# Kernel optimization log

Hardware: AMD Instinct MI355X
Metric: run time of the kernel (lower is better)

## Reference

```python
import jax, jax.numpy as jnp
import numpy as np

N = 100_000      # nodes
E = 500_000      # bonds
DN = 128         # dim_node_embedding
DB = 64          # dim_bond_embedding
NTOK = 4         # num_bond_token
DIN = 2 * DN + 2 * DB  # 384
LEAKY = 0.001
LN_EPS = 1e-5
DIST_MAX = 20.0
STEP = 0.5


def _lrelu(v):
    return jnp.where(v >= 0, v, LEAKY * v)


def _layernorm(v, w, b):
    m = v.mean(-1, keepdims=True)
    var = ((v - m) ** 2).mean(-1, keepdims=True)
    return (v - m) / jnp.sqrt(var + LN_EPS) * w + b


def setup_inputs() -> dict:
    key = jax.random.key(0)
    ks = jax.random.split(key, 20)
    x = jax.random.normal(ks[0], (N, 3), dtype=jnp.float32) * 3.0
    pos = jax.random.normal(ks[1], (N, 3), dtype=jnp.float32)
    node_embedding = jax.random.normal(ks[2], (N, DN), dtype=jnp.float32)
    i0 = jax.random.randint(ks[3], (E,), 0, N)
    off = jax.random.randint(ks[4], (E,), 1, N)  # nonzero -> no self-bonds
    bond_index = jnp.stack([i0, (i0 + off) % N], axis=1).astype(jnp.int32)
    bond_types = jax.random.randint(ks[5], (E,), 0, NTOK).astype(jnp.int32)
    s = 0.02
    params = dict(
        bond_emb=jax.random.normal(ks[6], (NTOK, DB), dtype=jnp.float32),
        W0=jax.random.normal(ks[7], (DIN, DN), dtype=jnp.float32) * s,
        b0=jnp.zeros((DN,), jnp.float32),
        W1=jax.random.normal(ks[8], (DN, DN), dtype=jnp.float32) * s,
        b1=jnp.zeros((DN,), jnp.float32),
        ln1_w=jnp.ones((DN,), jnp.float32),
        ln1_b=jnp.zeros((DN,), jnp.float32),
        W2=jax.random.normal(ks[9], (DN, DN), dtype=jnp.float32) * s,
        b2=jnp.zeros((DN,), jnp.float32),
        ln2_w=jnp.ones((DN,), jnp.float32),
        ln2_b=jnp.zeros((DN,), jnp.float32),
        Wo=jax.random.normal(ks[10], (DN, 2), dtype=jnp.float32) * s,
        bo=jnp.zeros((2,), jnp.float32),
    )
    return dict(x=x, pos=pos, node_embedding=node_embedding,
                bond_index=bond_index, bond_types=bond_types, **params)


def reference(x, pos, node_embedding, bond_index, bond_types,
              bond_emb, W0, b0, W1, b1, ln1_w, ln1_b,
              W2, b2, ln2_w, ln2_b, Wo, bo):
    i = bond_index[:, 0]
    j = bond_index[:, 1]

    # ---- BondLength geometry ----
    diff = x[i] - x[j]                                   # [E,3]
    dist = jnp.linalg.norm(diff, axis=-1, keepdims=True)  # [E,1]
    u = diff / dist                                       # [E,3] unit j->i? (i-j)/d
    direction = jnp.stack([u, -u], axis=-1)               # [E,3,2]

    # ---- Smearing (gaussian RBF + overflow bin, normalized) ----
    offset = jnp.linspace(0.0, DIST_MAX, DB - 1, dtype=jnp.float32)  # [63]
    delta = DIST_MAX / (DB - 2)
    coeff = -0.5 / (delta * delta)
    rbf = jnp.exp(coeff * (dist - offset) ** 2)            # [E,63]
    ovf = (dist >= DIST_MAX).astype(x.dtype)               # [E,1]
    smear = jnp.concatenate([rbf, ovf], axis=-1)           # [E,64]
    smear = smear / smear.sum(axis=-1, keepdims=True)

    # ---- Edge MLP (LeakyMLP, num_layer=2, dim_end=2) ----
    feat = jnp.concatenate(
        [node_embedding[i], node_embedding[j], bond_emb[bond_types], smear],
        axis=-1)                                           # [E,384]
    h = _lrelu(feat @ W0 + b0)
    h = _lrelu(_layernorm(h @ W1 + b1, ln1_w, ln1_b))
    h = _lrelu(_layernorm(h @ W2 + b2, ln2_w, ln2_b))
    force = h @ Wo + bo                                    # [E,2]

    # ---- position update (scatter-add) ----
    update = force[:, None, :] * direction                 # [E,3,2]
    pos = pos.at[i].add(STEP * update[..., 0])
    pos = pos.at[j].add(STEP * update[..., 1])
    return pos
```

## Files before the change

kernel.cpp:

```cpp
#include <hip/hip_runtime.h>
#include <stdint.h>

#define N_EDGES 500000
#define N_NODES 100000

typedef __attribute__((ext_vector_type(8))) short short8;
typedef __attribute__((ext_vector_type(4))) float floatx4;

__device__ __forceinline__ uint16_t f2bf(float f) {
  union { float f; uint32_t u; } cv; cv.f = f;
  uint32_t u = cv.u;
  return (uint16_t)((u + 0x7FFFu + ((u >> 16) & 1u)) >> 16);
}
__device__ __forceinline__ float bf2f(uint16_t h) {
  union { uint32_t u; float f; } cv; cv.u = ((uint32_t)h) << 16; return cv.f;
}
__device__ __forceinline__ float lrelu(float v) { return v >= 0.0f ? v : 0.001f * v; }

__global__ void prep0_kernel(const float* __restrict__ W0, const float* __restrict__ b0,
                             const float* __restrict__ W1, const float* __restrict__ W2,
                             const float* __restrict__ bemb,
                             uint16_t* __restrict__ w0ab, uint16_t* __restrict__ w0c,
                             uint16_t* __restrict__ w1f, uint16_t* __restrict__ w2f,
                             float* __restrict__ be0f) {
  int id = blockIdx.x * 256 + threadIdx.x;
  if (id < 32768) {
    int f = id;
    int j = f & 7, lane = (f >> 3) & 63, ntt = (f >> 9) & 15, ks = f >> 13;
    int k = ks * 32 + (lane >> 4) * 8 + j;
    int row = (ntt < 8) ? k : (128 + k);
    int col = (ntt & 7) * 16 + (lane & 15);
    w0ab[f] = f2bf(W0[row * 128 + col]);
  } else if (id < 40960) {
    int f = id - 32768;
    int j = f & 7, lane = (f >> 3) & 63, nt = (f >> 9) & 7, ks = f >> 12;
    int k = ks * 32 + (lane >> 4) * 8 + j;
    w0c[f] = f2bf(W0[(320 + k) * 128 + nt * 16 + (lane & 15)]);
  } else if (id < 57344) {
    int f = id - 40960;
    int j = f & 7, lane = (f >> 3) & 63, nt = (f >> 9) & 7, ks = f >> 12;
    int k = ks * 32 + (lane >> 4) * 8 + j;
    w1f[f] = f2bf(W1[k * 128 + nt * 16 + (lane & 15)]);
  } else if (id < 73728) {
    int f = id - 57344;
    int j = f & 7, lane = (f >> 3) & 63, nt = (f >> 9) & 7, ks = f >> 12;
    int k = ks * 32 + (lane >> 4) * 8 + j;
    w2f[f] = f2bf(W2[k * 128 + nt * 16 + (lane & 15)]);
  } else if (id < 74240) {
    int t = id - 73728; int ty = t >> 7, n = t & 127;
    float s = b0[n];
    for (int kk = 0; kk < 64; ++kk) s += bemb[ty * 64 + kk] * W0[(256 + kk) * 128 + n];
    be0f[t] = s;
  }
}

__launch_bounds__(256, 3)
__global__ void prep_p_kernel(const float* __restrict__ nemb, const uint16_t* __restrict__ w0ab,
                              uint16_t* __restrict__ Pa, uint16_t* __restrict__ Pb) {
  __shared__ __align__(16) uint16_t aLds[4 * 16 * 136];
  const int tid = threadIdx.x;
  const int lane = tid & 63;
  const int wave = tid >> 6;
  const int n15 = lane & 15;
  const int quad = lane >> 4;
  uint16_t* myA = aLds + wave * (16 * 136);
  const int base = blockIdx.x * 64 + wave * 16;

  {
    const int le = lane >> 2, sub = lane & 3;
    int r = base + le; if (r >= N_NODES) r = N_NODES - 1;
    const float4* src = (const float4*)(nemb + (size_t)r * 128);
#pragma unroll
    for (int g = 0; g < 4; ++g) {
      float4 a = src[sub * 8 + g * 2], b = src[sub * 8 + g * 2 + 1];
      uint4 pk;
      pk.x = f2bf(a.x) | ((uint32_t)f2bf(a.y) << 16);
      pk.y = f2bf(a.z) | ((uint32_t)f2bf(a.w) << 16);
      pk.z = f2bf(b.x) | ((uint32_t)f2bf(b.y) << 16);
      pk.w = f2bf(b.z) | ((uint32_t)f2bf(b.w) << 16);
      *(uint4*)(myA + le * 136 + sub * 32 + g * 8) = pk;
    }
  }

  floatx4 acc[16];
#pragma unroll
  for (int t = 0; t < 16; ++t) acc[t] = (floatx4){0.f, 0.f, 0.f, 0.f};
#pragma unroll
  for (int ks = 0; ks < 4; ++ks) {
    short8 a = *(const short8*)(myA + n15 * 136 + ks * 32 + quad * 8);
#pragma unroll
    for (int ntt = 0; ntt < 16; ++ntt) {
      short8 b = *(const short8*)(w0ab + ((ks * 16 + ntt) * 64 + lane) * 8);
      acc[ntt] = __builtin_amdgcn_mfma_f32_16x16x32_bf16(a, b, acc[ntt], 0, 0, 0);
    }
  }

#pragma unroll
  for (int p = 0; p < 2; ++p) {
#pragma unroll
    for (int nt = 0; nt < 8; ++nt)
#pragma unroll
      for (int r = 0; r < 4; ++r)
        myA[(quad * 4 + r) * 136 + nt * 16 + n15] = f2bf(acc[p * 8 + nt][r]);
    const int le = lane >> 2, sub = lane & 3;
    int row = base + le;
    if (row < N_NODES) {
      uint16_t* dst = (p == 0 ? Pa : Pb) + (size_t)row * 128;
#pragma unroll
      for (int g = 0; g < 4; ++g)
        *(uint4*)(dst + sub * 32 + g * 8) =
            *(const uint4*)(myA + le * 136 + sub * 32 + g * 8);
    }
  }
}

__global__ void copy_pos_kernel(const float* __restrict__ pos, float* __restrict__ out, int n) {
  int id = blockIdx.x * 256 + threadIdx.x;
  if (id < n) out[id] = pos[id];
}

template <int NKS>
__device__ __forceinline__ void gemm_fw(const uint16_t* __restrict__ wf,
                                        const uint16_t* aRow, int lane, floatx4* acc) {
#pragma unroll
  for (int ks = 0; ks < NKS; ++ks) {
    short8 a = *(const short8*)(aRow + ks * 32);
#pragma unroll
    for (int nt = 0; nt < 8; ++nt) {
      short8 b = *(const short8*)(wf + ((ks * 8 + nt) * 64 + lane) * 8);
      acc[nt] = __builtin_amdgcn_mfma_f32_16x16x32_bf16(a, b, acc[nt], 0, 0, 0);
    }
  }
}

__launch_bounds__(256, 3)
__global__ void bond_mlp_kernel(const float* __restrict__ x,
                                const int* __restrict__ bidx, const int* __restrict__ btyp,
                                const uint16_t* __restrict__ Pa, const uint16_t* __restrict__ Pb,
                                const uint16_t* __restrict__ w0c, const uint16_t* __restrict__ w1f,
                                const uint16_t* __restrict__ w2f, const float* __restrict__ be0f,
                                const float* __restrict__ b1, const float* __restrict__ ln1w,
                                const float* __restrict__ ln1b,
                                const float* __restrict__ b2, const float* __restrict__ ln2w,
                                const float* __restrict__ ln2b,
                                const float* __restrict__ Wo, const float* __restrict__ bo,
                                float* __restrict__ out) {
  __shared__ __align__(16) uint16_t wlds[4 * 5312];
  __shared__ float u_lds[64][3];
  __shared__ int ij_lds[64][2];
  __shared__ int type_lds[64];

  const int tid = threadIdx.x;
  const int lane = tid & 63;
  const int wave = tid >> 6;
  const int n15 = lane & 15;
  const int quad = lane >> 4;

  uint16_t* base16 = wlds + wave * 5312;
  float* h0pre = (float*)base16;
  uint16_t* hA = base16;
  uint16_t* smearA = base16 + 4160;

  {
    const int le = lane >> 2, sub = lane & 3;
    const int lrow = le;
    const int ge = blockIdx.x * 64 + wave * 16 + le;
    const bool valid = ge < N_EDGES;
    int vi = 0, vj = 0, bt = 0;
    if (valid) { vi = bidx[2 * ge]; vj = bidx[2 * ge + 1]; bt = btyp[ge]; }
    float dx, dy, dz;
    if (valid) {
      dx = x[3 * vi]     - x[3 * vj];
      dy = x[3 * vi + 1] - x[3 * vj + 1];
      dz = x[3 * vi + 2] - x[3 * vj + 2];
    } else { dx = 1.0f; dy = 0.0f; dz = 0.0f; }
    float dist = sqrtf(dx * dx + dy * dy + dz * dz);
    float rinv = 1.0f / dist;
    if (sub == 0) {
      int gr = wave * 16 + lrow;
      u_lds[gr][0] = dx * rinv; u_lds[gr][1] = dy * rinv; u_lds[gr][2] = dz * rinv;
      ij_lds[gr][0] = vi; ij_lds[gr][1] = vj; type_lds[gr] = bt;
    }
    const uint4* pa = (const uint4*)(Pa + (size_t)vi * 128);
    const uint4* pb = (const uint4*)(Pb + (size_t)vj * 128);
    const float4* bb = (const float4*)(be0f + bt * 128);
#pragma unroll
    for (int g = 0; g < 4; ++g) {
      uint4 av = pa[sub * 4 + g];
      uint4 bv = pb[sub * 4 + g];
      float4 e0 = bb[sub * 8 + g * 2], e1 = bb[sub * 8 + g * 2 + 1];
      float4 s0, s1;
      s0.x = bf2f((uint16_t)(av.x & 0xFFFF)) + bf2f((uint16_t)(bv.x & 0xFFFF)) + e0.x;
      s0.y = bf2f((uint16_t)(av.x >> 16))    + bf2f((uint16_t)(bv.x >> 16))    + e0.y;
      s0.z = bf2f((uint16_t)(av.y & 0xFFFF)) + bf2f((uint16_t)(bv.y & 0xFFFF)) + e0.z;
      s0.w = bf2f((uint16_t)(av.y >> 16))    + bf2f((uint16_t)(bv.y >> 16))    + e0.w;
      s1.x = bf2f((uint16_t)(av.z & 0xFFFF)) + bf2f((uint16_t)(bv.z & 0xFFFF)) + e1.x;
      s1.y = bf2f((uint16_t)(av.z >> 16))    + bf2f((uint16_t)(bv.z >> 16))    + e1.y;
      s1.z = bf2f((uint16_t)(av.w & 0xFFFF)) + bf2f((uint16_t)(bv.w & 0xFFFF)) + e1.z;
      s1.w = bf2f((uint16_t)(av.w >> 16))    + bf2f((uint16_t)(bv.w >> 16))    + e1.w;
      *(float4*)(h0pre + lrow * 130 + sub * 32 + g * 8) = s0;
      *(float4*)(h0pre + lrow * 130 + sub * 32 + g * 8 + 4) = s1;
    }
    const float delta = 20.0f / 62.0f;
    const float coeff = -0.5f / (delta * delta);
    float sv[16]; float ssum = 0.0f;
#pragma unroll
    for (int t = 0; t < 16; ++t) {
      int kk = sub * 16 + t;
      float v;
      if (kk < 63) { float d = dist - (float)kk * delta; v = __expf(coeff * d * d); }
      else v = (dist >= 20.0f) ? 1.0f : 0.0f;
      sv[t] = v; ssum += v;
    }
    ssum += __shfl_xor(ssum, 1);
    ssum += __shfl_xor(ssum, 2);
    float sinv = 1.0f / ssum;
#pragma unroll
    for (int g = 0; g < 2; ++g) {
      uint4 pk;
      pk.x = f2bf(sv[g*8+0]*sinv) | ((uint32_t)f2bf(sv[g*8+1]*sinv) << 16);
      pk.y = f2bf(sv[g*8+2]*sinv) | ((uint32_t)f2bf(sv[g*8+3]*sinv) << 16);
      pk.z = f2bf(sv[g*8+4]*sinv) | ((uint32_t)f2bf(sv[g*8+5]*sinv) << 16);
      pk.w = f2bf(sv[g*8+6]*sinv) | ((uint32_t)f2bf(sv[g*8+7]*sinv) << 16);
      *(uint4*)(smearA + lrow * 72 + sub * 16 + g * 8) = pk;
    }
  }

  floatx4 acc[8];
#pragma unroll
  for (int nt = 0; nt < 8; ++nt)
#pragma unroll
    for (int r = 0; r < 4; ++r)
      acc[nt][r] = h0pre[(quad * 4 + r) * 130 + nt * 16 + n15];

  gemm_fw<2>(w0c, smearA + n15 * 72 + quad * 8, lane, acc);

#pragma unroll
  for (int nt = 0; nt < 8; ++nt)
#pragma unroll
    for (int r = 0; r < 4; ++r)
      hA[(quad * 4 + r) * 136 + nt * 16 + n15] = f2bf(lrelu(acc[nt][r]));

#pragma unroll
  for (int nt = 0; nt < 8; ++nt) acc[nt] = (floatx4){0.f, 0.f, 0.f, 0.f};
  gemm_fw<4>(w1f, hA + n15 * 136 + quad * 8, lane, acc);

  {
    float bv[8], wv[8], bb2[8];
#pragma unroll
    for (int nt = 0; nt < 8; ++nt) {
      int col = nt * 16 + n15;
      bv[nt] = b1[col]; wv[nt] = ln1w[col]; bb2[nt] = ln1b[col];
    }
    float s[4] = {0,0,0,0}, q[4] = {0,0,0,0};
#pragma unroll
    for (int nt = 0; nt < 8; ++nt)
#pragma unroll
      for (int r = 0; r < 4; ++r) { float v = acc[nt][r] + bv[nt]; s[r] += v; q[r] += v * v; }
#pragma unroll
    for (int m = 1; m <= 8; m <<= 1)
#pragma unroll
      for (int r = 0; r < 4; ++r) { s[r] += __shfl_xor(s[r], m); q[r] += __shfl_xor(q[r], m); }
    float mean[4], rstd[4];
#pragma unroll
    for (int r = 0; r < 4; ++r) {
      mean[r] = s[r] * (1.0f / 128.0f);
      float var = q[r] * (1.0f / 128.0f) - mean[r] * mean[r];
      rstd[r] = rsqrtf(var + 1e-5f);
    }
#pragma unroll
    for (int nt = 0; nt < 8; ++nt)
#pragma unroll
      for (int r = 0; r < 4; ++r) {
        float v = acc[nt][r] + bv[nt];
        float vn = (v - mean[r]) * rstd[r] * wv[nt] + bb2[nt];
        hA[(quad * 4 + r) * 136 + nt * 16 + n15] = f2bf(lrelu(vn));
      }
  }

#pragma unroll
  for (int nt = 0; nt < 8; ++nt) acc[nt] = (floatx4){0.f, 0.f, 0.f, 0.f};
  gemm_fw<4>(w2f, hA + n15 * 136 + quad * 8, lane, acc);

  {
    float bv[8], wv[8], bb2[8], wo0[8], wo1[8];
#pragma unroll
    for (int nt = 0; nt < 8; ++nt) {
      int col = nt * 16 + n15;
      bv[nt] = b2[col]; wv[nt] = ln2w[col]; bb2[nt] = ln2b[col];
      wo0[nt] = Wo[2 * col]; wo1[nt] = Wo[2 * col + 1];
    }
    float s[4] = {0,0,0,0}, q[4] = {0,0,0,0};
#pragma unroll
    for (int nt = 0; nt < 8; ++nt)
#pragma unroll
      for (int r = 0; r < 4; ++r) { float v = acc[nt][r] + bv[nt]; s[r] += v; q[r] += v * v; }
#pragma unroll
    for (int m = 1; m <= 8; m <<= 1)
#pragma unroll
      for (int r = 0; r < 4; ++r) { s[r] += __shfl_xor(s[r], m); q[r] += __shfl_xor(q[r], m); }
    float mean[4], rstd[4];
#pragma unroll
    for (int r = 0; r < 4; ++r) {
      mean[r] = s[r] * (1.0f / 128.0f);
      float var = q[r] * (1.0f / 128.0f) - mean[r] * mean[r];
      rstd[r] = rsqrtf(var + 1e-5f);
    }
    float f0[4] = {0,0,0,0}, f1[4] = {0,0,0,0};
#pragma unroll
    for (int nt = 0; nt < 8; ++nt)
#pragma unroll
      for (int r = 0; r < 4; ++r) {
        float v = acc[nt][r] + bv[nt];
        float vn = lrelu((v - mean[r]) * rstd[r] * wv[nt] + bb2[nt]);
        f0[r] += vn * wo0[nt];
        f1[r] += vn * wo1[nt];
      }
#pragma unroll
    for (int m = 1; m <= 8; m <<= 1)
#pragma unroll
      for (int r = 0; r < 4; ++r) { f0[r] += __shfl_xor(f0[r], m); f1[r] += __shfl_xor(f1[r], m); }

    if (n15 < 4) {
      int gr = wave * 16 + quad * 4 + n15;
      int ge2 = blockIdx.x * 64 + gr;
      if (ge2 < N_EDGES) {
        float F0 = (n15 == 0) ? f0[0] : (n15 == 1) ? f0[1] : (n15 == 2) ? f0[2] : f0[3];
        float F1 = (n15 == 0) ? f1[0] : (n15 == 1) ? f1[1] : (n15 == 2) ? f1[2] : f1[3];
        F0 += bo[0]; F1 += bo[1];
        float ux = u_lds[gr][0], uy = u_lds[gr][1], uz = u_lds[gr][2];
        int ii = ij_lds[gr][0], jj = ij_lds[gr][1];
        float c0 = 0.5f * F0;
        float c1 = -0.5f * F1;
        atomicAdd(out + 3 * ii,     c0 * ux);
        atomicAdd(out + 3 * ii + 1, c0 * uy);
        atomicAdd(out + 3 * ii + 2, c0 * uz);
        atomicAdd(out + 3 * jj,     c1 * ux);
        atomicAdd(out + 3 * jj + 1, c1 * uy);
        atomicAdd(out + 3 * jj + 2, c1 * uz);
      }
    }
  }
}

extern "C" void kernel_launch(void* const* d_in, const int* in_sizes, int n_in,
                              void* d_out, int out_size, void* d_ws, size_t ws_size,
                              hipStream_t stream) {
  const float* x    = (const float*)d_in[0];
  const float* pos  = (const float*)d_in[1];
  const float* nemb = (const float*)d_in[2];
  const int*   bidx = (const int*)d_in[3];
  const int*   btyp = (const int*)d_in[4];
  const float* bemb = (const float*)d_in[5];
  const float* W0   = (const float*)d_in[6];
  const float* b0   = (const float*)d_in[7];
  const float* W1   = (const float*)d_in[8];
  const float* b1   = (const float*)d_in[9];
  const float* ln1w = (const float*)d_in[10];
  const float* ln1b = (const float*)d_in[11];
  const float* W2   = (const float*)d_in[12];
  const float* b2   = (const float*)d_in[13];
  const float* ln2w = (const float*)d_in[14];
  const float* ln2b = (const float*)d_in[15];
  const float* Wo   = (const float*)d_in[16];
  const float* bo   = (const float*)d_in[17];
  float* out = (float*)d_out;

  uint16_t* w0ab = (uint16_t*)d_ws;
  uint16_t* w0c  = w0ab + 32768;
  uint16_t* w1f  = w0c + 8192;
  uint16_t* w2f  = w1f + 16384;
  float*    be0f = (float*)(w2f + 16384);
  uint16_t* Pa   = (uint16_t*)(be0f + 512);
  uint16_t* Pb   = Pa + (size_t)N_NODES * 128;

  prep0_kernel<<<290, 256, 0, stream>>>(W0, b0, W1, W2, bemb, w0ab, w0c, w1f, w2f, be0f);
  prep_p_kernel<<<(N_NODES + 63) / 64, 256, 0, stream>>>(nemb, w0ab, Pa, Pb);
  copy_pos_kernel<<<(out_size + 255) / 256, 256, 0, stream>>>(pos, out, out_size);
  bond_mlp_kernel<<<(N_EDGES + 63) / 64, 256, 0, stream>>>(
      x, bidx, btyp, Pa, Pb, w0c, w1f, w2f, be0f,
      b1, ln1w, ln1b, b2, ln2w, ln2b, Wo, bo, out);
}
```

Measured before the change: 369.0 us.

## Use truncating bf16 packs, prefetch weight fragments, fuse pos copy into prep

Replaces round-to-nearest bf16 conversion with truncation via a byte-permute pack, and simplifies the bf16-to-float unpacks and leaky ReLU into cheaper ALU ops. The weight-fragment loads in the MFMA loops are hoisted and double-buffered so loads overlap the matrix instructions. The separate position-copy kernel is folded into the prep kernel, removing one launch. Truncation changes rounding, which slightly lowers accuracy, and the extra prefetch buffers raise register pressure.

Result: faster. 357.6 us (-3.1%).

```diff
diff --git a/kernel.cpp b/kernel.cpp
--- a/kernel.cpp
+++ b/kernel.cpp
@@ -12,17 +12,27 @@
   uint32_t u = cv.u;
   return (uint16_t)((u + 0x7FFFu + ((u >> 16) & 1u)) >> 16);
 }
-__device__ __forceinline__ float bf2f(uint16_t h) {
-  union { uint32_t u; float f; } cv; cv.u = ((uint32_t)h) << 16; return cv.f;
-}
-__device__ __forceinline__ float lrelu(float v) { return v >= 0.0f ? v : 0.001f * v; }
+__device__ __forceinline__ uint32_t pk2bf(float lo, float hi) {
+  return __builtin_amdgcn_perm(__float_as_uint(hi), __float_as_uint(lo), 0x07060302u);
+}
+__device__ __forceinline__ uint16_t bftrunc(float f) {
+  return (uint16_t)(__float_as_uint(f) >> 16);
+}
+__device__ __forceinline__ float bf2f_lo(uint32_t u) {
+  return __uint_as_float(u << 16);
+}
+__device__ __forceinline__ float bf2f_hi(uint32_t u) {
+  return __uint_as_float(u & 0xFFFF0000u);
+}
+__device__ __forceinline__ float lrelu(float v) { return fmaxf(v, 0.001f * v); }
 
 __global__ void prep0_kernel(const float* __restrict__ W0, const float* __restrict__ b0,
                              const float* __restrict__ W1, const float* __restrict__ W2,
                              const float* __restrict__ bemb,
                              uint16_t* __restrict__ w0ab, uint16_t* __restrict__ w0c,
                              uint16_t* __restrict__ w1f, uint16_t* __restrict__ w2f,
-                             float* __restrict__ be0f) {
+                             float* __restrict__ be0f,
+                             const float* __restrict__ pos, float* __restrict__ out, int npos) {
   int id = blockIdx.x * 256 + threadIdx.x;
   if (id < 32768) {
     int f = id;
@@ -51,6 +61,8 @@
     float s = b0[n];
     for (int kk = 0; kk < 64; ++kk) s += bemb[ty * 64 + kk] * W0[(256 + kk) * 128 + n];
     be0f[t] = s;
+  } else if (id - 74240 < npos) {
+    out[id - 74240] = pos[id - 74240];
   }
 }
 
@@ -74,10 +86,8 @@
     for (int g = 0; g < 4; ++g) {
       float4 a = src[sub * 8 + g * 2], b = src[sub * 8 + g * 2 + 1];
       uint4 pk;
-      pk.x = f2bf(a.x) | ((uint32_t)f2bf(a.y) << 16);
-      pk.y = f2bf(a.z) | ((uint32_t)f2bf(a.w) << 16);
-      pk.z = f2bf(b.x) | ((uint32_t)f2bf(b.y) << 16);
-      pk.w = f2bf(b.z) | ((uint32_t)f2bf(b.w) << 16);
+      pk.x = pk2bf(a.x, a.y); pk.y = pk2bf(a.z, a.w);
+      pk.z = pk2bf(b.x, b.y); pk.w = pk2bf(b.z, b.w);
       *(uint4*)(myA + le * 136 + sub * 32 + g * 8) = pk;
     }
   }
@@ -85,14 +95,16 @@
   floatx4 acc[16];
 #pragma unroll
   for (int t = 0; t < 16; ++t) acc[t] = (floatx4){0.f, 0.f, 0.f, 0.f};
+  const short8* wfv = (const short8*)w0ab + lane;
 #pragma unroll
   for (int ks = 0; ks < 4; ++ks) {
     short8 a = *(const short8*)(myA + n15 * 136 + ks * 32 + quad * 8);
-#pragma unroll
-    for (int ntt = 0; ntt < 16; ++ntt) {
-      short8 b = *(const short8*)(w0ab + ((ks * 16 + ntt) * 64 + lane) * 8);
-      acc[ntt] = __builtin_amdgcn_mfma_f32_16x16x32_bf16(a, b, acc[ntt], 0, 0, 0);
-    }
+    short8 b[16];
+#pragma unroll
+    for (int ntt = 0; ntt < 16; ++ntt) b[ntt] = wfv[(ks * 16 + ntt) * 64];
+#pragma unroll
+    for (int ntt = 0; ntt < 16; ++ntt)
+      acc[ntt] = __builtin_amdgcn_mfma_f32_16x16x32_bf16(a, b[ntt], acc[ntt], 0, 0, 0);
   }
 
 #pragma unroll
@@ -101,7 +113,7 @@
     for (int nt = 0; nt < 8; ++nt)
 #pragma unroll
       for (int r = 0; r < 4; ++r)
-        myA[(quad * 4 + r) * 136 + nt * 16 + n15] = f2bf(acc[p * 8 + nt][r]);
+        myA[(quad * 4 + r) * 136 + nt * 16 + n15] = bftrunc(acc[p * 8 + nt][r]);
     const int le = lane >> 2, sub = lane & 3;
     int row = base + le;
     if (row < N_NODES) {
@@ -114,22 +126,27 @@
   }
 }
 
-__global__ void copy_pos_kernel(const float* __restrict__ pos, float* __restrict__ out, int n) {
-  int id = blockIdx.x * 256 + threadIdx.x;
-  if (id < n) out[id] = pos[id];
-}
-
 template <int NKS>
 __device__ __forceinline__ void gemm_fw(const uint16_t* __restrict__ wf,
                                         const uint16_t* aRow, int lane, floatx4* acc) {
+  const short8* wfv = (const short8*)wf + lane;
+  short8 a[NKS];
+#pragma unroll
+  for (int ks = 0; ks < NKS; ++ks) a[ks] = *(const short8*)(aRow + ks * 32);
+  short8 b0[8], b1[8];
+#pragma unroll
+  for (int nt = 0; nt < 8; ++nt) b0[nt] = wfv[nt * 64];
 #pragma unroll
   for (int ks = 0; ks < NKS; ++ks) {
-    short8 a = *(const short8*)(aRow + ks * 32);
-#pragma unroll
-    for (int nt = 0; nt < 8; ++nt) {
-      short8 b = *(const short8*)(wf + ((ks * 8 + nt) * 64 + lane) * 8);
-      acc[nt] = __builtin_amdgcn_mfma_f32_16x16x32_bf16(a, b, acc[nt], 0, 0, 0);
-    }
+    const short8* cur = (ks & 1) ? b1 : b0;
+    short8* nxt = (ks & 1) ? b0 : b1;
+    if (ks + 1 < NKS) {
+#pragma unroll
+      for (int nt = 0; nt < 8; ++nt) nxt[nt] = wfv[((ks + 1) * 8 + nt) * 64];
+    }
+#pragma unroll
+    for (int nt = 0; nt < 8; ++nt)
+      acc[nt] = __builtin_amdgcn_mfma_f32_16x16x32_bf16(a[ks], cur[nt], acc[nt], 0, 0, 0);
   }
 }
 
@@ -183,21 +200,21 @@
     }
     const uint4* pa = (const uint4*)(Pa + (size_t)vi * 128);
     const uint4* pb = (const uint4*)(Pb + (size_t)vj * 128);
-    const float4* bb = (const float4*)(be0f + bt * 128);
+    const float4* bbp = (const float4*)(be0f + bt * 128);
 #pragma unroll
     for (int g = 0; g < 4; ++g) {
       uint4 av = pa[sub * 4 + g];
       uint4 bv = pb[sub * 4 + g];
-      float4 e0 = bb[sub * 8 + g * 2], e1 = bb[sub * 8 + g * 2 + 1];
+      float4 e0 = bbp[sub * 8 + g * 2], e1 = bbp[sub * 8 + g * 2 + 1];
       float4 s0, s1;
-      s0.x = bf2f((uint16_t)(av.x & 0xFFFF)) + bf2f((uint16_t)(bv.x & 0xFFFF)) + e0.x;
-      s0.y = bf2f((uint16_t)(av.x >> 16))    + bf2f((uint16_t)(bv.x >> 16))    + e0.y;
-      s0.z = bf2f((uint16_t)(av.y & 0xFFFF)) + bf2f((uint16_t)(bv.y & 0xFFFF)) + e0.z;
-      s0.w = bf2f((uint16_t)(av.y >> 16))    + bf2f((uint16_t)(bv.y >> 16))    + e0.w;
-      s1.x = bf2f((uint16_t)(av.z & 0xFFFF)) + bf2f((uint16_t)(bv.z & 0xFFFF)) + e1.x;
-      s1.y = bf2f((uint16_t)(av.z >> 16))    + bf2f((uint16_t)(bv.z >> 16))    + e1.y;
-      s1.z = bf2f((uint16_t)(av.w & 0xFFFF)) + bf2f((uint16_t)(bv.w & 0xFFFF)) + e1.z;
-      s1.w = bf2f((uint16_t)(av.w >> 16))    + bf2f((uint16_t)(bv.w >> 16))    + e1.w;
+      s0.x = bf2f_lo(av.x) + bf2f_lo(bv.x) + e0.x;
+      s0.y = bf2f_hi(av.x) + bf2f_hi(bv.x) + e0.y;
+      s0.z = bf2f_lo(av.y) + bf2f_lo(bv.y) + e0.z;
+      s0.w = bf2f_hi(av.y) + bf2f_hi(bv.y) + e0.w;
+      s1.x = bf2f_lo(av.z) + bf2f_lo(bv.z) + e1.x;
+      s1.y = bf2f_hi(av.z) + bf2f_hi(bv.z) + e1.y;
+      s1.z = bf2f_lo(av.w) + bf2f_lo(bv.w) + e1.z;
+      s1.w = bf2f_hi(av.w) + bf2f_hi(bv.w) + e1.w;
       *(float4*)(h0pre + lrow * 130 + sub * 32 + g * 8) = s0;
       *(float4*)(h0pre + lrow * 130 + sub * 32 + g * 8 + 4) = s1;
     }
@@ -218,10 +235,10 @@
 #pragma unroll
     for (int g = 0; g < 2; ++g) {
       uint4 pk;
-      pk.x = f2bf(sv[g*8+0]*sinv) | ((uint32_t)f2bf(sv[g*8+1]*sinv) << 16);
-      pk.y = f2bf(sv[g*8+2]*sinv) | ((uint32_t)f2bf(sv[g*8+3]*sinv) << 16);
-      pk.z = f2bf(sv[g*8+4]*sinv) | ((uint32_t)f2bf(sv[g*8+5]*sinv) << 16);
-      pk.w = f2bf(sv[g*8+6]*sinv) | ((uint32_t)f2bf(sv[g*8+7]*sinv) << 16);
+      pk.x = pk2bf(sv[g*8+0]*sinv, sv[g*8+1]*sinv);
+      pk.y = pk2bf(sv[g*8+2]*sinv, sv[g*8+3]*sinv);
+      pk.z = pk2bf(sv[g*8+4]*sinv, sv[g*8+5]*sinv);
+      pk.w = pk2bf(sv[g*8+6]*sinv, sv[g*8+7]*sinv);
       *(uint4*)(smearA + lrow * 72 + sub * 16 + g * 8) = pk;
     }
   }
@@ -239,7 +256,7 @@
   for (int nt = 0; nt < 8; ++nt)
 #pragma unroll
     for (int r = 0; r < 4; ++r)
-      hA[(quad * 4 + r) * 136 + nt * 16 + n15] = f2bf(lrelu(acc[nt][r]));
+      hA[(quad * 4 + r) * 136 + nt * 16 + n15] = bftrunc(lrelu(acc[nt][r]));
 
 #pragma unroll
   for (int nt = 0; nt < 8; ++nt) acc[nt] = (floatx4){0.f, 0.f, 0.f, 0.f};
@@ -274,7 +291,7 @@
       for (int r = 0; r < 4; ++r) {
         float v = acc[nt][r] + bv[nt];
         float vn = (v - mean[r]) * rstd[r] * wv[nt] + bb2[nt];
-        hA[(quad * 4 + r) * 136 + nt * 16 + n15] = f2bf(lrelu(vn));
+        hA[(quad * 4 + r) * 136 + nt * 16 + n15] = bftrunc(lrelu(vn));
       }
   }
 
@@ -374,9 +391,9 @@
   uint16_t* Pa   = (uint16_t*)(be0f + 512);
   uint16_t* Pb   = Pa + (size_t)N_NODES * 128;
 
-  prep0_kernel<<<290, 256, 0, stream>>>(W0, b0, W1, W2, bemb, w0ab, w0c, w1f, w2f, be0f);
+  prep0_kernel<<<(74240 + out_size + 255) / 256, 256, 0, stream>>>(
+      W0, b0, W1, W2, bemb, w0ab, w0c, w1f, w2f, be0f, pos, out, out_size);
   prep_p_kernel<<<(N_NODES + 63) / 64, 256, 0, stream>>>(nemb, w0ab, Pa, Pb);
-  copy_pos_kernel<<<(out_size + 255) / 256, 256, 0, stream>>>(pos, out, out_size);
   bond_mlp_kernel<<<(N_EDGES + 63) / 64, 256, 0, stream>>>(
       x, bidx, btyp, Pa, Pb, w0c, w1f, w2f, be0f,
       b1, ln1w, ln1b, b2, ln2w, ln2b, Wo, bo, out);
```
